# Performance work log

Hardware: AMD Instinct MI355X
Metric: run time of the kernel (lower is better)

The kernel has to match this reference:

```python
import jax, jax.numpy as jnp
import numpy as np

L, D, H, G, HS, I, V, B, T = 4, 1024, 16, 4, 64, 2816, 32000, 4, 512
THETA = 10000.0
EPS = 1e-6


def setup_inputs() -> dict:
    key = jax.random.key(0)
    ks = jax.random.split(key, 10)
    s = 0.02
    return {
        "input_ids": jax.random.randint(ks[0], (B, T), 0, V),
        "embed": jax.random.normal(ks[1], (V, D)) * s,      # tied with lm_head
        "q_w": jax.random.normal(ks[2], (L, D, D)) * s,     # torch Linear: [out, in]
        "q_b": jax.random.normal(ks[3], (L, D)) * s,
        "kv_w": jax.random.normal(ks[4], (L, 2 * G * HS, D)) * s,
        "kv_b": jax.random.normal(ks[5], (L, 2 * G * HS)) * s,
        "o_w": jax.random.normal(ks[6], (L, D, D)) * s,
        "ln1_w": jnp.ones((L, D)),
        "ln2_w": jnp.ones((L, D)),
        "gate_w": jax.random.normal(ks[7], (L, I, D)) * s,
        "up_w": jax.random.normal(ks[8], (L, I, D)) * s,
        "down_w": jax.random.normal(ks[9], (L, D, I)) * s,
        "last_w": jnp.ones((D,)),
    }


def rms_norm(x, w):
    return x * jax.lax.rsqrt(jnp.mean(x * x, axis=-1, keepdims=True) + EPS) * w


def rope_tables(t, hs):
    inv_freq = 1.0 / (THETA ** (jnp.arange(0, hs, 2, dtype=jnp.float32) / hs))
    ang = jnp.arange(t, dtype=jnp.float32)[:, None] * inv_freq[None, :]  # [T, hs/2]
    emb = jnp.concatenate([ang, ang], axis=-1)                           # [T, hs]
    return jnp.cos(emb), jnp.sin(emb)


def rotate_half(x):
    x1, x2 = jnp.split(x, 2, axis=-1)
    return jnp.concatenate([-x2, x1], axis=-1)


def reference(input_ids, embed, q_w, q_b, kv_w, kv_b, o_w, ln1_w, ln2_w, gate_w, up_w, down_w, last_w):
    x = embed[input_ids]  # [B, T, D]
    cos, sin = rope_tables(T, HS)                    # [T, HS] (buffers, const)
    c, s_ = cos[None, None], sin[None, None]         # [1, 1, T, HS]
    causal = jnp.tril(jnp.ones((T, T), dtype=bool))
    scale = 1.0 / np.sqrt(HS).astype(np.float32)
    for l in range(L):
        h = rms_norm(x, ln1_w[l])
        q = (h @ q_w[l].T + q_b[l]).reshape(B, T, H, HS).transpose(0, 2, 1, 3)  # bhtd
        kv = h @ kv_w[l].T + kv_b[l]
        k, v = jnp.split(kv, 2, axis=-1)
        k = k.reshape(B, T, G, HS).transpose(0, 2, 1, 3)  # bgtd
        v = v.reshape(B, T, G, HS).transpose(0, 2, 1, 3)
        k = jnp.repeat(k, H // G, axis=1)  # GQA kv repeat -> bhtd
        v = jnp.repeat(v, H // G, axis=1)
        q = q * c + rotate_half(q) * s_
        k = k * c + rotate_half(k) * s_
        attn = jnp.einsum('bhtd,bhsd->bhts', q, k) * scale
        attn = jnp.where(causal, attn, -jnp.inf)
        attn = jax.nn.softmax(attn, axis=-1)
        o = jnp.einsum('bhts,bhsd->bhtd', attn, v).transpose(0, 2, 1, 3).reshape(B, T, D)
        x = x + o @ o_w[l].T  # o_proj has no bias
        h = rms_norm(x, ln2_w[l])
        x = x + (jax.nn.silu(h @ gate_w[l].T) * (h @ up_w[l].T)) @ down_w[l].T  # SwiGLU
    x = rms_norm(x, last_w)
    return x @ embed.T  # tied lm_head -> logits [B, T, V]
```

## Files before the change

### kernel.cpp

```cpp
#include <hip/hip_runtime.h>
#include <hip/hip_bf16.h>
#include <stdint.h>


typedef __bf16 bf16x8 __attribute__((ext_vector_type(8)));
typedef __bf16 bf16x4 __attribute__((ext_vector_type(4)));
typedef float  f32x4  __attribute__((ext_vector_type(4)));

#define AS1 __attribute__((address_space(1)))
#define AS3 __attribute__((address_space(3)))

__device__ __forceinline__ void gld_lds16(const void* g, void* l) {
  __builtin_amdgcn_global_load_lds((const AS1 void*)g, (AS3 void*)l, 16, 0, 0);
}

__global__ __launch_bounds__(256) void cvt_kernel(const float* __restrict__ in,
                                                  __bf16* __restrict__ out, int n4) {
  for (int i = blockIdx.x * 256 + threadIdx.x; i < n4; i += gridDim.x * 256) {
    f32x4 v = __builtin_nontemporal_load(&((const f32x4*)in)[i]);
    bf16x4 o;
#pragma unroll
    for (int j = 0; j < 4; ++j) o[j] = (__bf16)v[j];
    ((bf16x4*)out)[i] = o;
  }
}

__global__ __launch_bounds__(256) void embed_kernel(const int* __restrict__ ids,
                                                    const float* __restrict__ emb,
                                                    float* __restrict__ x) {
  const int tok = blockIdx.x;
  const float* src = emb + (size_t)ids[tok] * 1024;
  float* dst = x + (size_t)tok * 1024;
#pragma unroll
  for (int j = 0; j < 4; ++j) {
    const int d = threadIdx.x + j * 256;
    dst[d] = src[d];
  }
}

__global__ __launch_bounds__(256) void rmsnorm_kernel(const float* __restrict__ x,
                                                      const float* __restrict__ wgt,
                                                      __bf16* __restrict__ out) {
  const int row = blockIdx.x;
  const float* xr = x + (size_t)row * 1024;
  float v[4];
  float ss = 0.f;
#pragma unroll
  for (int j = 0; j < 4; ++j) { v[j] = xr[threadIdx.x + j * 256]; ss += v[j] * v[j]; }
#pragma unroll
  for (int m = 1; m < 64; m <<= 1) ss += __shfl_xor(ss, m, 64);
  __shared__ float red[4];
  if ((threadIdx.x & 63) == 0) red[threadIdx.x >> 6] = ss;
  __syncthreads();
  const float tot = red[0] + red[1] + red[2] + red[3];
  const float sc = rsqrtf(tot * (1.f / 1024.f) + 1e-6f);
#pragma unroll
  for (int j = 0; j < 4; ++j) {
    const int d = threadIdx.x + j * 256;
    out[(size_t)row * 1024 + d] = (__bf16)(v[j] * sc * wgt[d]);
  }
}

#define GEMM_PREAMBLE                                              \
  const int t = threadIdx.x;                                       \
  const int lane = t & 63;                                         \
  const int w = t >> 6, wr = w >> 1, wc = w & 1;                   \
  const int lr = lane & 15;                                        \
  const int lk = (lane >> 4) * 8;                                  \
  const int sr = t >> 2;                                           \
  const int scol = (t & 3) * 8;

#define FLAT_SWZ(BMC, BNC)                                         \
  const int chunk_ = (int)(gridDim.x >> 3);                        \
  const int wg_ = (blockIdx.x & 7) * chunk_ + (blockIdx.x >> 3);   \
  const int bm = wg_ % (BMC);                                      \
  const int rest_ = wg_ / (BMC);                                   \
  const int bn = rest_ % (BNC);                                    \
  const int ks = rest_ / (BNC);                                    \
  (void)ks;

#define GEMM_FRAGS_MFMA                                            \
  bf16x8 af[4], bfr[4];                                            \
  _Pragma("unroll") for (int m = 0; m < 4; ++m)                    \
    af[m] = *(const bf16x8*)&As[(wr * 64 + m * 16 + lr) * 32 + lk];\
  _Pragma("unroll") for (int n = 0; n < 4; ++n)                    \
    bfr[n] = *(const bf16x8*)&Bs[(wc * 64 + n * 16 + lr) * 32 + lk];\
  _Pragma("unroll") for (int m = 0; m < 4; ++m)                    \
    _Pragma("unroll") for (int n = 0; n < 4; ++n)                  \
      acc[m][n] = __builtin_amdgcn_mfma_f32_16x16x32_bf16(af[m], bfr[n], acc[m][n], 0, 0, 0);

template <int EPI, int BMC, int BNC, int KSP>
__global__ __launch_bounds__(256) void gemm_bt(const __bf16* __restrict__ A,
                                               const __bf16* __restrict__ Bb,
                                               float* __restrict__ Cf,
                                               int K, int ldc) {
  __shared__ __bf16 As[128 * 32];
  __shared__ __bf16 Bs[128 * 32];
  GEMM_PREAMBLE
  FLAT_SWZ(BMC, BNC)
  const int klen = K / KSP;
  const int kbeg = ks * klen;

  const __bf16* a0 = A + (size_t)(bm * 128 + sr) * K + scol;
  const __bf16* a1 = A + (size_t)(bm * 128 + 64 + sr) * K + scol;
  const __bf16* bb0 = Bb + (size_t)(bn * 128 + sr) * K + scol;
  const __bf16* bb1 = Bb + (size_t)(bn * 128 + 64 + sr) * K + scol;

  f32x4 acc[4][4] = {};
  for (int k0 = kbeg; k0 < kbeg + klen; k0 += 32) {
    gld_lds16(a0 + k0, &As[t * 8]);
    gld_lds16(a1 + k0, &As[2048 + t * 8]);
    gld_lds16(bb0 + k0, &Bs[t * 8]);
    gld_lds16(bb1 + k0, &Bs[2048 + t * 8]);
    __syncthreads();
    GEMM_FRAGS_MFMA
    __syncthreads();
  }
  const int r0 = bm * 128 + wr * 64 + (lane >> 4) * 4;
  const int c0 = bn * 128 + wc * 64 + lr;
#pragma unroll
  for (int m = 0; m < 4; ++m)
#pragma unroll
    for (int r = 0; r < 4; ++r) {
      const size_t rowoff = (size_t)(r0 + m * 16 + r) * ldc;
#pragma unroll
      for (int n = 0; n < 4; ++n) {
        if (EPI == 3) Cf[rowoff + c0 + n * 16] = acc[m][n][r];
        else          atomicAdd(&Cf[rowoff + c0 + n * 16], acc[m][n][r]);
      }
    }
}

__global__ __launch_bounds__(256) void qkv_gemm(const __bf16* __restrict__ A,
                                                const __bf16* __restrict__ qw,
                                                const __bf16* __restrict__ kvw,
                                                const float* __restrict__ q_b,
                                                const float* __restrict__ kv_b,
                                                __bf16* __restrict__ qb,
                                                __bf16* __restrict__ kvb) {
  const int K = 1024;
  __shared__ __bf16 As[128 * 32];
  __shared__ __bf16 Bs[128 * 32];
  GEMM_PREAMBLE
  FLAT_SWZ(16, 12)
  const bool isq = bn < 8;
  const int bnn = isq ? bn : bn - 8;
  const __bf16* Bw = (isq ? qw : kvw) + (size_t)(bnn * 128) * K;

  const __bf16* a0 = A + (size_t)(bm * 128 + sr) * K + scol;
  const __bf16* a1 = A + (size_t)(bm * 128 + 64 + sr) * K + scol;
  const __bf16* bb0 = Bw + (size_t)sr * K + scol;
  const __bf16* bb1 = Bw + (size_t)(64 + sr) * K + scol;

  f32x4 acc[4][4] = {};
  for (int k0 = 0; k0 < K; k0 += 32) {
    gld_lds16(a0 + k0, &As[t * 8]);
    gld_lds16(a1 + k0, &As[2048 + t * 8]);
    gld_lds16(bb0 + k0, &Bs[t * 8]);
    gld_lds16(bb1 + k0, &Bs[2048 + t * 8]);
    __syncthreads();
    GEMM_FRAGS_MFMA
    __syncthreads();
  }

  const int ldc = isq ? 1024 : 512;
  __bf16* out = isq ? qb : kvb;
  const float* bias = isq ? q_b : kv_b;
  const int cb = bnn * 128 + wc * 64;
  const bool dorope = isq || (cb < 256);
  float bv[4];
#pragma unroll
  for (int n = 0; n < 4; ++n) bv[n] = bias[cb + n * 16 + lr];
  float inv0 = __expf((float)lr * -0.28782313662425574f);
  float inv1 = __expf((float)(16 + lr) * -0.28782313662425574f);

  const int r0 = bm * 128 + wr * 64 + (lane >> 4) * 4;
#pragma unroll
  for (int m = 0; m < 4; ++m)
#pragma unroll
    for (int r = 0; r < 4; ++r) {
      const int row = r0 + m * 16 + r;
      float c4[4];
#pragma unroll
      for (int n = 0; n < 4; ++n) c4[n] = acc[m][n][r] + bv[n];
      if (dorope) {
        const float pos = (float)(row & 511);
        float sg, cg;
        __sincosf(pos * inv0, &sg, &cg);
        float x1 = c4[0], x2 = c4[2];
        c4[0] = x1 * cg - x2 * sg;
        c4[2] = x2 * cg + x1 * sg;
        __sincosf(pos * inv1, &sg, &cg);
        x1 = c4[1]; x2 = c4[3];
        c4[1] = x1 * cg - x2 * sg;
        c4[3] = x2 * cg + x1 * sg;
      }
      const size_t rowoff = (size_t)row * ldc;
#pragma unroll
      for (int n = 0; n < 4; ++n) out[rowoff + cb + n * 16 + lr] = (__bf16)c4[n];
    }
}

__global__ __launch_bounds__(256) void gateup_gemm(const __bf16* __restrict__ A,
                                                   const __bf16* __restrict__ gw,
                                                   const __bf16* __restrict__ uw,
                                                   __bf16* __restrict__ gbuf,
                                                   __bf16* __restrict__ ubuf) {
  const int K = 1024;
  __shared__ __bf16 As[128 * 32];
  __shared__ __bf16 Bs[128 * 32];
  GEMM_PREAMBLE
  FLAT_SWZ(16, 44)
  const bool isg = bn < 22;
  const int bnn = isg ? bn : bn - 22;
  const __bf16* Bw = (isg ? gw : uw) + (size_t)(bnn * 128) * K;
  __bf16* out = isg ? gbuf : ubuf;

  const __bf16* a0 = A + (size_t)(bm * 128 + sr) * K + scol;
  const __bf16* a1 = A + (size_t)(bm * 128 + 64 + sr) * K + scol;
  const __bf16* bb0 = Bw + (size_t)sr * K + scol;
  const __bf16* bb1 = Bw + (size_t)(64 + sr) * K + scol;

  f32x4 acc[4][4] = {};
  for (int k0 = 0; k0 < K; k0 += 32) {
    gld_lds16(a0 + k0, &As[t * 8]);
    gld_lds16(a1 + k0, &As[2048 + t * 8]);
    gld_lds16(bb0 + k0, &Bs[t * 8]);
    gld_lds16(bb1 + k0, &Bs[2048 + t * 8]);
    __syncthreads();
    GEMM_FRAGS_MFMA
    __syncthreads();
  }
  const int r0 = bm * 128 + wr * 64 + (lane >> 4) * 4;
  const int c0 = bnn * 128 + wc * 64 + lr;
#pragma unroll
  for (int m = 0; m < 4; ++m)
#pragma unroll
    for (int r = 0; r < 4; ++r) {
      const size_t rowoff = (size_t)(r0 + m * 16 + r) * 2816;
#pragma unroll
      for (int n = 0; n < 4; ++n) out[rowoff + c0 + n * 16] = (__bf16)acc[m][n][r];
    }
}

__global__ __launch_bounds__(256) void down_gemm(const __bf16* __restrict__ g,
                                                 const __bf16* __restrict__ u,
                                                 const __bf16* __restrict__ Bb,
                                                 float* __restrict__ Cf) {
  const int K = 2816;
  __shared__ __bf16 As[128 * 32];
  __shared__ __bf16 Bs[128 * 32];
  GEMM_PREAMBLE
  FLAT_SWZ(16, 8)
  const int klen = 704;
  const int kbeg = ks * klen;

  const size_t arow0 = (size_t)(bm * 128 + sr) * K + scol;
  const size_t arow1 = (size_t)(bm * 128 + 64 + sr) * K + scol;
  const __bf16* bb0 = Bb + (size_t)(bn * 128 + sr) * K + scol;
  const __bf16* bb1 = Bb + (size_t)(bn * 128 + 64 + sr) * K + scol;

  f32x4 acc[4][4] = {};
  for (int k0 = kbeg; k0 < kbeg + klen; k0 += 32) {
    {
      bf16x8 gv0 = *(const bf16x8*)(g + arow0 + k0);
      bf16x8 uv0 = *(const bf16x8*)(u + arow0 + k0);
      bf16x8 gv1 = *(const bf16x8*)(g + arow1 + k0);
      bf16x8 uv1 = *(const bf16x8*)(u + arow1 + k0);
      bf16x8 s0, s1;
#pragma unroll
      for (int j = 0; j < 8; ++j) {
        const float gf = (float)gv0[j];
        s0[j] = (__bf16)(gf / (1.f + __expf(-gf)) * (float)uv0[j]);
      }
#pragma unroll
      for (int j = 0; j < 8; ++j) {
        const float gf = (float)gv1[j];
        s1[j] = (__bf16)(gf / (1.f + __expf(-gf)) * (float)uv1[j]);
      }
      *(bf16x8*)&As[t * 8] = s0;
      *(bf16x8*)&As[2048 + t * 8] = s1;
    }
    gld_lds16(bb0 + k0, &Bs[t * 8]);
    gld_lds16(bb1 + k0, &Bs[2048 + t * 8]);
    __syncthreads();
    GEMM_FRAGS_MFMA
    __syncthreads();
  }
  const int r0 = bm * 128 + wr * 64 + (lane >> 4) * 4;
  const int c0 = bn * 128 + wc * 64 + lr;
#pragma unroll
  for (int m = 0; m < 4; ++m)
#pragma unroll
    for (int r = 0; r < 4; ++r) {
      const size_t rowoff = (size_t)(r0 + m * 16 + r) * 1024;
#pragma unroll
      for (int n = 0; n < 4; ++n) atomicAdd(&Cf[rowoff + c0 + n * 16], acc[m][n][r]);
    }
}

__global__ __launch_bounds__(512, 2) void lmhead_gemm(const __bf16* __restrict__ A,
                                                      const __bf16* __restrict__ Bb,
                                                      float* __restrict__ C) {
  __shared__ __bf16 lds[2][4][8192];
  const int t = threadIdx.x;
  const int lane = t & 63;
  const int w = t >> 6;
  const int wr = w >> 2;
  const int wc = w & 3;
  const int lr = lane & 15;
  const int lg = lane >> 4;
  const int sx = (lr & 7) << 4;

  const int wg = (blockIdx.x & 7) * 125 + (blockIdx.x >> 3);
  const int bm = wg & 7;
  const int bn = wg >> 3;

  int srow[2], scol[2];
#pragma unroll
  for (int j = 0; j < 2; ++j) {
    const int q = (t + j * 512) * 16;
    const int row = q >> 7;
    const int p = q ^ ((row & 7) << 4);
    srow[j] = row;
    scol[j] = (p & 127) >> 1;
  }

  auto STAGE = [&](int buf, int kt) {
#pragma unroll
    for (int ht = 0; ht < 4; ++ht) {
      const __bf16* base = (ht < 2)
          ? A + (size_t)(bm * 256 + ht * 128) * 1024
          : Bb + (size_t)(bn * 256 + (ht - 2) * 128) * 1024;
#pragma unroll
      for (int j = 0; j < 2; ++j) {
        gld_lds16(base + (size_t)srow[j] * 1024 + kt * 64 + scol[j],
                  (char*)&lds[buf][ht][0] + (size_t)(t + j * 512) * 16);
      }
    }
  };

  STAGE(0, 0);
  STAGE(1, 1);

  f32x4 acc[8][4] = {};
  for (int kt = 0; kt < 16; ++kt) {
    const int cur = kt & 1;
    if (kt < 15) asm volatile("s_waitcnt vmcnt(8)" ::: "memory");
    else         asm volatile("s_waitcnt vmcnt(0)" ::: "memory");
    __builtin_amdgcn_s_barrier();

    const char* Ab = (const char*)&lds[cur][wr][0];
    const char* Bbs = (const char*)&lds[cur][2 + (wc >> 1)][0];
    const int rB0 = (wc & 1) * 64;

    bf16x8 af[8][2];
#pragma unroll
    for (int mi = 0; mi < 8; ++mi)
#pragma unroll
      for (int ksl = 0; ksl < 2; ++ksl) {
        const int row = mi * 16 + lr;
        af[mi][ksl] = *(const bf16x8*)(Ab + ((row * 128 + ksl * 64 + lg * 16) ^ sx));
      }
#pragma unroll
    for (int np = 0; np < 2; ++np) {
      bf16x8 bfr[2][2];
#pragma unroll
      for (int ni = 0; ni < 2; ++ni)
#pragma unroll
        for (int ksl = 0; ksl < 2; ++ksl) {
          const int row = rB0 + (np * 2 + ni) * 16 + lr;
          bfr[ni][ksl] = *(const bf16x8*)(Bbs + ((row * 128 + ksl * 64 + lg * 16) ^ sx));
        }
      __builtin_amdgcn_s_setprio(1);
#pragma unroll
      for (int mi = 0; mi < 8; ++mi)
#pragma unroll
        for (int ni = 0; ni < 2; ++ni)
#pragma unroll
          for (int ksl = 0; ksl < 2; ++ksl)
            acc[mi][np * 2 + ni] = __builtin_amdgcn_mfma_f32_16x16x32_bf16(
                af[mi][ksl], bfr[ni][ksl], acc[mi][np * 2 + ni], 0, 0, 0);
      __builtin_amdgcn_s_setprio(0);
    }
    asm volatile("s_waitcnt lgkmcnt(0)" ::: "memory");
    __builtin_amdgcn_s_barrier();
    if (kt + 2 < 16) STAGE(cur, kt + 2);
  }

  const int r0 = bm * 256 + wr * 128 + lg * 4;
  const int c0 = bn * 256 + wc * 64 + lr;
#pragma unroll
  for (int m = 0; m < 8; ++m)
#pragma unroll
    for (int r = 0; r < 4; ++r) {
      float* crow = C + (size_t)(r0 + m * 16 + r) * 32000 + c0;
#pragma unroll
      for (int n = 0; n < 4; ++n)
        __builtin_nontemporal_store(acc[m][n][r], crow + n * 16);
    }
}

__global__ __launch_bounds__(256) void attn_kernel(const __bf16* __restrict__ q,
                                                   const __bf16* __restrict__ kv,
                                                   __bf16* __restrict__ o) {
  const int qt = blockIdx.x, hh = blockIdx.y, b = blockIdx.z;
  const int g = hh >> 2;
  const int t = threadIdx.x, lane = t & 63, w = t >> 6;
  const int lr = lane & 15, lg = lane >> 4;

  __shared__ __bf16 Vt[64 * 72];
  __shared__ __bf16 Ps[64 * 72];

  bf16x8 qa[2];
  {
    const size_t qoff = ((size_t)(b * 512 + qt * 64 + w * 16 + lr)) * 1024 + hh * 64;
    qa[0] = *(const bf16x8*)(q + qoff + lg * 8);
    qa[1] = *(const bf16x8*)(q + qoff + 32 + lg * 8);
  }

  f32x4 acc_o[4] = {};
  float mrow[4], lrow[4];
#pragma unroll
  for (int r = 0; r < 4; ++r) { mrow[r] = -1e30f; lrow[r] = 0.f; }

  const int srow = t >> 3;
  const int sdv = (t & 7) * 8;

  for (int kt = 0; kt <= qt; ++kt) {
    const size_t krow = ((size_t)(b * 512 + kt * 64 + srow)) * 512;

    bf16x8 kb[4][2];
#pragma unroll
    for (int nf = 0; nf < 4; ++nf)
#pragma unroll
      for (int kc = 0; kc < 2; ++kc)
        kb[nf][kc] = *(const bf16x8*)(kv +
            ((size_t)(b * 512 + kt * 64 + nf * 16 + lr)) * 512 + g * 64 + kc * 32 + lg * 8);

    {
      const __bf16* vsrc = kv + krow + 256 + g * 64 + sdv;
      bf16x8 v0 = *(const bf16x8*)vsrc;
      bf16x8 v1 = *(const bf16x8*)(vsrc + 32 * 512);
#pragma unroll
      for (int j = 0; j < 8; ++j) Vt[(sdv + j) * 72 + srow] = v0[j];
#pragma unroll
      for (int j = 0; j < 8; ++j) Vt[(sdv + j) * 72 + srow + 32] = v1[j];
    }
    __syncthreads();

    f32x4 s[4] = {};
#pragma unroll
    for (int nf = 0; nf < 4; ++nf)
#pragma unroll
      for (int kc = 0; kc < 2; ++kc)
        s[nf] = __builtin_amdgcn_mfma_f32_16x16x32_bf16(qa[kc], kb[nf][kc], s[nf], 0, 0, 0);

    float pm[4][4], mx[4];
    const int qg = qt * 64 + w * 16 + lg * 4;
    const int kg = kt * 64 + lr;
#pragma unroll
    for (int r = 0; r < 4; ++r) mx[r] = -1e30f;
#pragma unroll
    for (int nf = 0; nf < 4; ++nf)
#pragma unroll
      for (int r = 0; r < 4; ++r) {
        float vv = s[nf][r] * 0.125f;
        vv = (kg + nf * 16 <= qg + r) ? vv : -1e30f;
        pm[nf][r] = vv;
        mx[r] = fmaxf(mx[r], vv);
      }
#pragma unroll
    for (int msk = 1; msk < 16; msk <<= 1)
#pragma unroll
      for (int r = 0; r < 4; ++r) mx[r] = fmaxf(mx[r], __shfl_xor(mx[r], msk, 64));

    float rs[4];
#pragma unroll
    for (int r = 0; r < 4; ++r) {
      const float mn = fmaxf(mrow[r], mx[r]);
      const float f = __expf(mrow[r] - mn);
      mrow[r] = mn;
      lrow[r] *= f;
#pragma unroll
      for (int df = 0; df < 4; ++df) acc_o[df][r] *= f;
      float rsum = 0.f;
#pragma unroll
      for (int nf = 0; nf < 4; ++nf) {
        const float pp = __expf(pm[nf][r] - mn);
        pm[nf][r] = pp;
        rsum += pp;
      }
      rs[r] = rsum;
    }
#pragma unroll
    for (int msk = 1; msk < 16; msk <<= 1)
#pragma unroll
      for (int r = 0; r < 4; ++r) rs[r] += __shfl_xor(rs[r], msk, 64);
#pragma unroll
    for (int r = 0; r < 4; ++r) lrow[r] += rs[r];

#pragma unroll
    for (int nf = 0; nf < 4; ++nf)
#pragma unroll
      for (int r = 0; r < 4; ++r)
        Ps[(w * 16 + lg * 4 + r) * 72 + nf * 16 + lr] = (__bf16)pm[nf][r];

#pragma unroll
    for (int df = 0; df < 4; ++df)
#pragma unroll
      for (int kc = 0; kc < 2; ++kc) {
        bf16x8 pa = *(const bf16x8*)&Ps[(w * 16 + lr) * 72 + kc * 32 + lg * 8];
        bf16x8 vb = *(const bf16x8*)&Vt[(df * 16 + lr) * 72 + kc * 32 + lg * 8];
        acc_o[df] = __builtin_amdgcn_mfma_f32_16x16x32_bf16(pa, vb, acc_o[df], 0, 0, 0);
      }
    __syncthreads();
  }

#pragma unroll
  for (int df = 0; df < 4; ++df)
#pragma unroll
    for (int r = 0; r < 4; ++r) {
      const int trow = qt * 64 + w * 16 + lg * 4 + r;
      o[((size_t)(b * 512 + trow)) * 1024 + hh * 64 + df * 16 + lr] =
          (__bf16)(acc_o[df][r] / lrow[r]);
    }
}

extern "C" void kernel_launch(void* const* d_in, const int* in_sizes, int n_in,
                              void* d_out, int out_size, void* d_ws, size_t ws_size,
                              hipStream_t stream) {
  const int* ids = (const int*)d_in[0];
  const float* emb_f = (const float*)d_in[1];
  const float* qw_f = (const float*)d_in[2];
  const float* q_b = (const float*)d_in[3];
  const float* kvw_f = (const float*)d_in[4];
  const float* kv_b = (const float*)d_in[5];
  const float* ow_f = (const float*)d_in[6];
  const float* ln1 = (const float*)d_in[7];
  const float* ln2 = (const float*)d_in[8];
  const float* gw_f = (const float*)d_in[9];
  const float* uw_f = (const float*)d_in[10];
  const float* dw_f = (const float*)d_in[11];
  const float* lw = (const float*)d_in[12];
  float* out = (float*)d_out;

  char* p = (char*)d_ws;
  float* x = (float*)p;        p += (size_t)2048 * 1024 * 4;
  __bf16* h = (__bf16*)p;      p += (size_t)2048 * 1024 * 2;
  __bf16* qb = (__bf16*)p;     p += (size_t)2048 * 1024 * 2;
  __bf16* kvb = (__bf16*)p;    p += (size_t)2048 * 512 * 2;
  __bf16* ao = (__bf16*)p;     p += (size_t)2048 * 1024 * 2;
  __bf16* gb = (__bf16*)p;     p += (size_t)2048 * 2816 * 2;
  __bf16* ub = (__bf16*)p;     p += (size_t)2048 * 2816 * 2;
  __bf16* emb_b = (__bf16*)p;  p += (size_t)32000 * 1024 * 2;
  __bf16* qw_b = (__bf16*)p;   p += (size_t)4 * 1024 * 1024 * 2;
  __bf16* kvw_b = (__bf16*)p;  p += (size_t)4 * 512 * 1024 * 2;
  __bf16* ow_b = (__bf16*)p;   p += (size_t)4 * 1024 * 1024 * 2;
  __bf16* gw_b = (__bf16*)p;   p += (size_t)4 * 2816 * 1024 * 2;
  __bf16* uw_b = (__bf16*)p;   p += (size_t)4 * 2816 * 1024 * 2;
  __bf16* dw_b = (__bf16*)p;   p += (size_t)4 * 2816 * 1024 * 2;

  cvt_kernel<<<2048, 256, 0, stream>>>(emb_f, emb_b, 32000 * 1024 / 4);
  cvt_kernel<<<1024, 256, 0, stream>>>(qw_f, qw_b, 4 * 1024 * 1024 / 4);
  cvt_kernel<<<1024, 256, 0, stream>>>(kvw_f, kvw_b, 4 * 512 * 1024 / 4);
  cvt_kernel<<<1024, 256, 0, stream>>>(ow_f, ow_b, 4 * 1024 * 1024 / 4);
  cvt_kernel<<<1024, 256, 0, stream>>>(gw_f, gw_b, 4 * 2816 * 1024 / 4);
  cvt_kernel<<<1024, 256, 0, stream>>>(uw_f, uw_b, 4 * 2816 * 1024 / 4);
  cvt_kernel<<<1024, 256, 0, stream>>>(dw_f, dw_b, 4 * 2816 * 1024 / 4);

  embed_kernel<<<2048, 256, 0, stream>>>(ids, emb_f, x);
  for (int l = 0; l < 4; ++l) {
    rmsnorm_kernel<<<2048, 256, 0, stream>>>(x, ln1 + l * 1024, h);
    qkv_gemm<<<192, 256, 0, stream>>>(
        h, qw_b + (size_t)l * 1024 * 1024, kvw_b + (size_t)l * 512 * 1024,
        q_b + l * 1024, kv_b + l * 512, qb, kvb);
    attn_kernel<<<dim3(8, 16, 4), 256, 0, stream>>>(qb, kvb, ao);
    gemm_bt<4, 16, 8, 4><<<512, 256, 0, stream>>>(
        ao, ow_b + (size_t)l * 1024 * 1024, x, 1024, 1024);
    rmsnorm_kernel<<<2048, 256, 0, stream>>>(x, ln2 + l * 1024, h);
    gateup_gemm<<<704, 256, 0, stream>>>(
        h, gw_b + (size_t)l * 2816 * 1024, uw_b + (size_t)l * 2816 * 1024, gb, ub);
    down_gemm<<<512, 256, 0, stream>>>(
        gb, ub, dw_b + (size_t)l * 1024 * 2816, x);
  }
  rmsnorm_kernel<<<2048, 256, 0, stream>>>(x, lw, h);
  lmhead_gemm<<<1000, 512, 0, stream>>>(h, emb_b, out);
}
```

Measured before the change: 998.7 us.

## Use K=64 XOR-swizzled LDS tiles in qkv/oproj/gateup GEMMs and fuse weight conversion

The qkv, o-proj and gate/up GEMMs now stage 64-wide K tiles instead of 32, with an XOR swizzle on LDS addresses to avoid bank conflicts. This halves the number of barrier pairs per K loop and gives the MFMA loop more work per synchronisation. The seven fp32-to-bf16 weight conversion launches are merged into one cvt_all kernel to cut launch overhead. LDS use per block doubles, which may lower occupancy, and the branchy index dispatch in cvt_all adds a little per-element cost.

```diff
diff --git a/kernel.cpp b/kernel.cpp
--- a/kernel.cpp
+++ b/kernel.cpp
@@ -14,14 +14,37 @@
   __builtin_amdgcn_global_load_lds((const AS1 void*)g, (AS3 void*)l, 16, 0, 0);
 }
 
-__global__ __launch_bounds__(256) void cvt_kernel(const float* __restrict__ in,
-                                                  __bf16* __restrict__ out, int n4) {
-  for (int i = blockIdx.x * 256 + threadIdx.x; i < n4; i += gridDim.x * 256) {
-    f32x4 v = __builtin_nontemporal_load(&((const f32x4*)in)[i]);
-    bf16x4 o;
-#pragma unroll
-    for (int j = 0; j < 4; ++j) o[j] = (__bf16)v[j];
-    ((bf16x4*)out)[i] = o;
+__device__ __forceinline__ void cvt4(const float* __restrict__ s, __bf16* __restrict__ d, int i) {
+  f32x4 v = __builtin_nontemporal_load(&((const f32x4*)s)[i]);
+  bf16x4 o;
+#pragma unroll
+  for (int j = 0; j < 4; ++j) o[j] = (__bf16)v[j];
+  ((bf16x4*)d)[i] = o;
+}
+
+__global__ __launch_bounds__(256) void cvt_all(
+    const float* __restrict__ e, __bf16* __restrict__ eb,
+    const float* __restrict__ qw, __bf16* __restrict__ qwb,
+    const float* __restrict__ kvw, __bf16* __restrict__ kvwb,
+    const float* __restrict__ ow, __bf16* __restrict__ owb,
+    const float* __restrict__ gw, __bf16* __restrict__ gwb,
+    const float* __restrict__ uw, __bf16* __restrict__ uwb,
+    const float* __restrict__ dw, __bf16* __restrict__ dwb) {
+  const int C0 = 8192000;
+  const int C1 = C0 + 1048576;
+  const int C2 = C1 + 524288;
+  const int C3 = C2 + 1048576;
+  const int C4 = C3 + 2883584;
+  const int C5 = C4 + 2883584;
+  const int C6 = C5 + 2883584;
+  for (int i = blockIdx.x * 256 + threadIdx.x; i < C6; i += gridDim.x * 256) {
+    if (i < C0)      cvt4(e, eb, i);
+    else if (i < C1) cvt4(qw, qwb, i - C0);
+    else if (i < C2) cvt4(kvw, kvwb, i - C1);
+    else if (i < C3) cvt4(ow, owb, i - C2);
+    else if (i < C4) cvt4(gw, gwb, i - C3);
+    else if (i < C5) cvt4(uw, uwb, i - C4);
+    else             cvt4(dw, dwb, i - C5);
   }
 }
 
@@ -61,73 +84,85 @@
   }
 }
 
-#define GEMM_PREAMBLE                                              \
-  const int t = threadIdx.x;                                       \
-  const int lane = t & 63;                                         \
-  const int w = t >> 6, wr = w >> 1, wc = w & 1;                   \
-  const int lr = lane & 15;                                        \
-  const int lk = (lane >> 4) * 8;                                  \
-  const int sr = t >> 2;                                           \
-  const int scol = (t & 3) * 8;
-
-#define FLAT_SWZ(BMC, BNC)                                         \
-  const int chunk_ = (int)(gridDim.x >> 3);                        \
-  const int wg_ = (blockIdx.x & 7) * chunk_ + (blockIdx.x >> 3);   \
-  const int bm = wg_ % (BMC);                                      \
-  const int rest_ = wg_ / (BMC);                                   \
-  const int bn = rest_ % (BNC);                                    \
-  const int ks = rest_ / (BNC);                                    \
-  (void)ks;
-
-#define GEMM_FRAGS_MFMA                                            \
-  bf16x8 af[4], bfr[4];                                            \
-  _Pragma("unroll") for (int m = 0; m < 4; ++m)                    \
-    af[m] = *(const bf16x8*)&As[(wr * 64 + m * 16 + lr) * 32 + lk];\
-  _Pragma("unroll") for (int n = 0; n < 4; ++n)                    \
-    bfr[n] = *(const bf16x8*)&Bs[(wc * 64 + n * 16 + lr) * 32 + lk];\
-  _Pragma("unroll") for (int m = 0; m < 4; ++m)                    \
-    _Pragma("unroll") for (int n = 0; n < 4; ++n)                  \
-      acc[m][n] = __builtin_amdgcn_mfma_f32_16x16x32_bf16(af[m], bfr[n], acc[m][n], 0, 0, 0);
-
-template <int EPI, int BMC, int BNC, int KSP>
-__global__ __launch_bounds__(256) void gemm_bt(const __bf16* __restrict__ A,
-                                               const __bf16* __restrict__ Bb,
-                                               float* __restrict__ Cf,
-                                               int K, int ldc) {
-  __shared__ __bf16 As[128 * 32];
-  __shared__ __bf16 Bs[128 * 32];
-  GEMM_PREAMBLE
-  FLAT_SWZ(BMC, BNC)
-  const int klen = K / KSP;
-  const int kbeg = ks * klen;
-
-  const __bf16* a0 = A + (size_t)(bm * 128 + sr) * K + scol;
-  const __bf16* a1 = A + (size_t)(bm * 128 + 64 + sr) * K + scol;
-  const __bf16* bb0 = Bb + (size_t)(bn * 128 + sr) * K + scol;
-  const __bf16* bb1 = Bb + (size_t)(bn * 128 + 64 + sr) * K + scol;
+#define GEMM64_PRE                                                  \
+  const int t = threadIdx.x;                                        \
+  const int lane = t & 63;                                          \
+  const int w = t >> 6, wr = w >> 1, wc = w & 1;                    \
+  const int lr = lane & 15;                                         \
+  const int lg = lane >> 4;                                         \
+  const int sx = (lr & 7) << 4;                                     \
+  int srow[4], scol[4];                                             \
+  _Pragma("unroll") for (int j = 0; j < 4; ++j) {                   \
+    const int q_ = (t + j * 256) * 16;                              \
+    const int row_ = q_ >> 7;                                       \
+    const int p_ = q_ ^ ((row_ & 7) << 4);                          \
+    srow[j] = row_; scol[j] = (p_ & 127) >> 1;                      \
+  }
+
+#define STAGE64(base, Kd, ldsb, k0)                                 \
+  _Pragma("unroll") for (int j = 0; j < 4; ++j)                     \
+    gld_lds16((base) + (size_t)srow[j] * (Kd) + (k0) + scol[j],     \
+              (char*)(ldsb) + (size_t)(t + j * 256) * 16);
+
+#define GEMM64_FRAGS_MFMA                                           \
+  bf16x8 af[4][2], bfr[4][2];                                       \
+  _Pragma("unroll") for (int m = 0; m < 4; ++m)                     \
+    _Pragma("unroll") for (int ks = 0; ks < 2; ++ks) {              \
+      const int row_ = wr * 64 + m * 16 + lr;                       \
+      af[m][ks] = *(const bf16x8*)((char*)As +                      \
+          ((row_ * 128 + ks * 64 + lg * 16) ^ sx));                 \
+    }                                                               \
+  _Pragma("unroll") for (int n = 0; n < 4; ++n)                     \
+    _Pragma("unroll") for (int ks = 0; ks < 2; ++ks) {              \
+      const int row_ = wc * 64 + n * 16 + lr;                       \
+      bfr[n][ks] = *(const bf16x8*)((char*)Bs +                     \
+          ((row_ * 128 + ks * 64 + lg * 16) ^ sx));                 \
+    }                                                               \
+  _Pragma("unroll") for (int m = 0; m < 4; ++m)                     \
+    _Pragma("unroll") for (int n = 0; n < 4; ++n)                   \
+      _Pragma("unroll") for (int ks = 0; ks < 2; ++ks)              \
+        acc[m][n] = __builtin_amdgcn_mfma_f32_16x16x32_bf16(        \
+            af[m][ks], bfr[n][ks], acc[m][n], 0, 0, 0);
+
+#define FLAT_SWZ(BMC, BNC)                                          \
+  const int chunk_ = (int)(gridDim.x >> 3);                         \
+  const int wg_ = (blockIdx.x & 7) * chunk_ + (blockIdx.x >> 3);    \
+  const int bm = wg_ % (BMC);                                       \
+  const int rest_ = wg_ / (BMC);                                    \
+  const int bn = rest_ % (BNC);                                     \
+  const int ks_ = rest_ / (BNC);                                    \
+  (void)ks_;
+
+__global__ __launch_bounds__(256) void oproj_gemm(const __bf16* __restrict__ A,
+                                                  const __bf16* __restrict__ Bb,
+                                                  float* __restrict__ Cf) {
+  const int K = 1024;
+  __shared__ __bf16 As[128 * 64];
+  __shared__ __bf16 Bs[128 * 64];
+  GEMM64_PRE
+  FLAT_SWZ(16, 8)
+  const int kbeg = ks_ * 256;
+
+  const __bf16* a0 = A + (size_t)(bm * 128) * K;
+  const __bf16* b0 = Bb + (size_t)(bn * 128) * K;
 
   f32x4 acc[4][4] = {};
-  for (int k0 = kbeg; k0 < kbeg + klen; k0 += 32) {
-    gld_lds16(a0 + k0, &As[t * 8]);
-    gld_lds16(a1 + k0, &As[2048 + t * 8]);
-    gld_lds16(bb0 + k0, &Bs[t * 8]);
-    gld_lds16(bb1 + k0, &Bs[2048 + t * 8]);
-    __syncthreads();
-    GEMM_FRAGS_MFMA
-    __syncthreads();
-  }
-  const int r0 = bm * 128 + wr * 64 + (lane >> 4) * 4;
+  for (int k0 = kbeg; k0 < kbeg + 256; k0 += 64) {
+    STAGE64(a0, K, As, k0)
+    STAGE64(b0, K, Bs, k0)
+    __syncthreads();
+    GEMM64_FRAGS_MFMA
+    __syncthreads();
+  }
+  const int r0 = bm * 128 + wr * 64 + lg * 4;
   const int c0 = bn * 128 + wc * 64 + lr;
 #pragma unroll
   for (int m = 0; m < 4; ++m)
 #pragma unroll
     for (int r = 0; r < 4; ++r) {
-      const size_t rowoff = (size_t)(r0 + m * 16 + r) * ldc;
-#pragma unroll
-      for (int n = 0; n < 4; ++n) {
-        if (EPI == 3) Cf[rowoff + c0 + n * 16] = acc[m][n][r];
-        else          atomicAdd(&Cf[rowoff + c0 + n * 16], acc[m][n][r]);
-      }
+      const size_t rowoff = (size_t)(r0 + m * 16 + r) * 1024;
+#pragma unroll
+      for (int n = 0; n < 4; ++n) atomicAdd(&Cf[rowoff + c0 + n * 16], acc[m][n][r]);
     }
 }
 
@@ -139,27 +174,21 @@
                                                 __bf16* __restrict__ qb,
                                                 __bf16* __restrict__ kvb) {
   const int K = 1024;
-  __shared__ __bf16 As[128 * 32];
-  __shared__ __bf16 Bs[128 * 32];
-  GEMM_PREAMBLE
+  __shared__ __bf16 As[128 * 64];
+  __shared__ __bf16 Bs[128 * 64];
+  GEMM64_PRE
   FLAT_SWZ(16, 12)
   const bool isq = bn < 8;
   const int bnn = isq ? bn : bn - 8;
   const __bf16* Bw = (isq ? qw : kvw) + (size_t)(bnn * 128) * K;
-
-  const __bf16* a0 = A + (size_t)(bm * 128 + sr) * K + scol;
-  const __bf16* a1 = A + (size_t)(bm * 128 + 64 + sr) * K + scol;
-  const __bf16* bb0 = Bw + (size_t)sr * K + scol;
-  const __bf16* bb1 = Bw + (size_t)(64 + sr) * K + scol;
+  const __bf16* a0 = A + (size_t)(bm * 128) * K;
 
   f32x4 acc[4][4] = {};
-  for (int k0 = 0; k0 < K; k0 += 32) {
-    gld_lds16(a0 + k0, &As[t * 8]);
-    gld_lds16(a1 + k0, &As[2048 + t * 8]);
-    gld_lds16(bb0 + k0, &Bs[t * 8]);
-    gld_lds16(bb1 + k0, &Bs[2048 + t * 8]);
-    __syncthreads();
-    GEMM_FRAGS_MFMA
+  for (int k0 = 0; k0 < K; k0 += 64) {
+    STAGE64(a0, K, As, k0)
+    STAGE64(Bw, K, Bs, k0)
+    __syncthreads();
+    GEMM64_FRAGS_MFMA
     __syncthreads();
   }
 
@@ -174,7 +203,7 @@
   float inv0 = __expf((float)lr * -0.28782313662425574f);
   float inv1 = __expf((float)(16 + lr) * -0.28782313662425574f);
 
-  const int r0 = bm * 128 + wr * 64 + (lane >> 4) * 4;
+  const int r0 = bm * 128 + wr * 64 + lg * 4;
 #pragma unroll
   for (int m = 0; m < 4; ++m)
 #pragma unroll
@@ -207,31 +236,25 @@
                                                    __bf16* __restrict__ gbuf,
                                                    __bf16* __restrict__ ubuf) {
   const int K = 1024;
-  __shared__ __bf16 As[128 * 32];
-  __shared__ __bf16 Bs[128 * 32];
-  GEMM_PREAMBLE
+  __shared__ __bf16 As[128 * 64];
+  __shared__ __bf16 Bs[128 * 64];
+  GEMM64_PRE
   FLAT_SWZ(16, 44)
   const bool isg = bn < 22;
   const int bnn = isg ? bn : bn - 22;
   const __bf16* Bw = (isg ? gw : uw) + (size_t)(bnn * 128) * K;
   __bf16* out = isg ? gbuf : ubuf;
-
-  const __bf16* a0 = A + (size_t)(bm * 128 + sr) * K + scol;
-  const __bf16* a1 = A + (size_t)(bm * 128 + 64 + sr) * K + scol;
-  const __bf16* bb0 = Bw + (size_t)sr * K + scol;
-  const __bf16* bb1 = Bw + (size_t)(64 + sr) * K + scol;
+  const __bf16* a0 = A + (size_t)(bm * 128) * K;
 
   f32x4 acc[4][4] = {};
-  for (int k0 = 0; k0 < K; k0 += 32) {
-    gld_lds16(a0 + k0, &As[t * 8]);
-    gld_lds16(a1 + k0, &As[2048 + t * 8]);
-    gld_lds16(bb0 + k0, &Bs[t * 8]);
-    gld_lds16(bb1 + k0, &Bs[2048 + t * 8]);
-    __syncthreads();
-    GEMM_FRAGS_MFMA
-    __syncthreads();
-  }
-  const int r0 = bm * 128 + wr * 64 + (lane >> 4) * 4;
+  for (int k0 = 0; k0 < K; k0 += 64) {
+    STAGE64(a0, K, As, k0)
+    STAGE64(Bw, K, Bs, k0)
+    __syncthreads();
+    GEMM64_FRAGS_MFMA
+    __syncthreads();
+  }
+  const int r0 = bm * 128 + wr * 64 + lg * 4;
   const int c0 = bnn * 128 + wc * 64 + lr;
 #pragma unroll
   for (int m = 0; m < 4; ++m)
@@ -242,6 +265,15 @@
       for (int n = 0; n < 4; ++n) out[rowoff + c0 + n * 16] = (__bf16)acc[m][n][r];
     }
 }
+
+#define GEMM_PREAMBLE32                                            \
+  const int t = threadIdx.x;                                       \
+  const int lane = t & 63;                                         \
+  const int w = t >> 6, wr = w >> 1, wc = w & 1;                   \
+  const int lr = lane & 15;                                        \
+  const int lk = (lane >> 4) * 8;                                  \
+  const int sr = t >> 2;                                           \
+  const int scol = (t & 3) * 8;
 
 __global__ __launch_bounds__(256) void down_gemm(const __bf16* __restrict__ g,
                                                  const __bf16* __restrict__ u,
@@ -250,10 +282,10 @@
   const int K = 2816;
   __shared__ __bf16 As[128 * 32];
   __shared__ __bf16 Bs[128 * 32];
-  GEMM_PREAMBLE
+  GEMM_PREAMBLE32
   FLAT_SWZ(16, 8)
   const int klen = 704;
-  const int kbeg = ks * klen;
+  const int kbeg = ks_ * klen;
 
   const size_t arow0 = (size_t)(bm * 128 + sr) * K + scol;
   const size_t arow1 = (size_t)(bm * 128 + 64 + sr) * K + scol;
@@ -284,7 +316,18 @@
     gld_lds16(bb0 + k0, &Bs[t * 8]);
     gld_lds16(bb1 + k0, &Bs[2048 + t * 8]);
     __syncthreads();
-    GEMM_FRAGS_MFMA
+    {
+      bf16x8 af[4], bfr[4];
+#pragma unroll
+      for (int m = 0; m < 4; ++m) af[m] = *(const bf16x8*)&As[(wr * 64 + m * 16 + lr) * 32 + lk];
+#pragma unroll
+      for (int n = 0; n < 4; ++n) bfr[n] = *(const bf16x8*)&Bs[(wc * 64 + n * 16 + lr) * 32 + lk];
+#pragma unroll
+      for (int m = 0; m < 4; ++m)
+#pragma unroll
+        for (int n = 0; n < 4; ++n)
+          acc[m][n] = __builtin_amdgcn_mfma_f32_16x16x32_bf16(af[m], bfr[n], acc[m][n], 0, 0, 0);
+    }
     __syncthreads();
   }
   const int r0 = bm * 128 + wr * 64 + (lane >> 4) * 4;
@@ -561,13 +604,8 @@
   __bf16* uw_b = (__bf16*)p;   p += (size_t)4 * 2816 * 1024 * 2;
   __bf16* dw_b = (__bf16*)p;   p += (size_t)4 * 2816 * 1024 * 2;
 
-  cvt_kernel<<<2048, 256, 0, stream>>>(emb_f, emb_b, 32000 * 1024 / 4);
-  cvt_kernel<<<1024, 256, 0, stream>>>(qw_f, qw_b, 4 * 1024 * 1024 / 4);
-  cvt_kernel<<<1024, 256, 0, stream>>>(kvw_f, kvw_b, 4 * 512 * 1024 / 4);
-  cvt_kernel<<<1024, 256, 0, stream>>>(ow_f, ow_b, 4 * 1024 * 1024 / 4);
-  cvt_kernel<<<1024, 256, 0, stream>>>(gw_f, gw_b, 4 * 2816 * 1024 / 4);
-  cvt_kernel<<<1024, 256, 0, stream>>>(uw_f, uw_b, 4 * 2816 * 1024 / 4);
-  cvt_kernel<<<1024, 256, 0, stream>>>(dw_f, dw_b, 4 * 2816 * 1024 / 4);
+  cvt_all<<<4096, 256, 0, stream>>>(emb_f, emb_b, qw_f, qw_b, kvw_f, kvw_b,
+                                    ow_f, ow_b, gw_f, gw_b, uw_f, uw_b, dw_f, dw_b);
 
   embed_kernel<<<2048, 256, 0, stream>>>(ids, emb_f, x);
   for (int l = 0; l < 4; ++l) {
@@ -576,8 +614,7 @@
         h, qw_b + (size_t)l * 1024 * 1024, kvw_b + (size_t)l * 512 * 1024,
         q_b + l * 1024, kv_b + l * 512, qb, kvb);
     attn_kernel<<<dim3(8, 16, 4), 256, 0, stream>>>(qb, kvb, ao);
-    gemm_bt<4, 16, 8, 4><<<512, 256, 0, stream>>>(
-        ao, ow_b + (size_t)l * 1024 * 1024, x, 1024, 1024);
+    oproj_gemm<<<512, 256, 0, stream>>>(ao, ow_b + (size_t)l * 1024 * 1024, x);
     rmsnorm_kernel<<<2048, 256, 0, stream>>>(x, ln2 + l * 1024, h);
     gateup_gemm<<<704, 256, 0, stream>>>(
         h, gw_b + (size_t)l * 2816 * 1024, uw_b + (size_t)l * 2816 * 1024, gb, ub);
```

Measured after the change: 996.8 us. No clear change (-0.2%).
